# Kernel optimization log

Measured on AMD Instinct MI355X. Metric: run time of the kernel, lower is better.

The kernel has to match this reference:

```python
import jax, jax.numpy as jnp
import numpy as np

B, T, C, NH = 1, 2048, 1024, 16
HS = C // NH            # 64
LEVEL = 6
LMIN = 2 ** LEVEL       # 64 (tail block size)
NB = T // LMIN          # 32 complete sets


def setup_inputs() -> dict:
    key = jax.random.key(0)
    ks = jax.random.split(key, 8)
    def w(k, shape, fan_in):
        return jax.random.normal(k, shape, jnp.float32) / np.sqrt(fan_in)
    return {
        "x": jax.random.normal(ks[0], (B, T, C), jnp.float32),
        "Wq": w(ks[1], (C, C), C),
        "Wk": w(ks[2], (C, C), C),
        "Wv": w(ks[3], (C, C), C),
        "Wkmap": w(ks[4], (HS, HS * HS), HS * HS),
        "bkmap": jnp.zeros((HS,), jnp.float32),
        "Wvmap": w(ks[5], (HS, HS * HS), HS * HS),
        "bvmap": jnp.zeros((HS,), jnp.float32),
        "Wc": w(ks[6], (C, C), C),
        "bc": jnp.zeros((C,), jnp.float32),
    }


def reference(x, Wq, Wk, Wv, Wkmap, bkmap, Wvmap, bvmap, Wc, bc):
    phi = lambda t: jax.nn.elu(t) + 1.0  # feature_map='elu'
    # preprocess: projections + feature map (no q/k normalization)
    q = phi((x @ Wq.T).reshape(B, T, NH, HS))
    k = phi((x @ Wk.T).reshape(B, T, NH, HS))
    v = (x @ Wv.T).reshape(B, T, NH, HS)

    # per-position outer products k_t (x) v_t, grouped into LMIN-sized blocks
    op = jnp.einsum('bthd,bthe->bthde', k, v).reshape(B, NB, LMIN, NH, HS, HS)
    # set feature = final state of linear-attn recurrence over each full block
    set_f = op.sum(axis=2).reshape(B, NB, NH, HS * HS)            # [B,NB,NH,HS^2]
    # tail feature at t = state over [t - t%LMIN, t] = in-block prefix cumsum
    tail_f = jnp.cumsum(op, axis=2).reshape(B, T, NH, HS * HS)    # [B,T,NH,HS^2]

    K = set_f @ Wkmap.T + bkmap      # [B,NB,NH,HS] (k_mapping=True)
    V = set_f @ Wvmap.T + bvmap      # [B,NB,NH,HS] (v_mapping=True)
    K_tail = tail_f @ Wkmap.T + bkmap  # [B,T,NH,HS]
    V_tail = tail_f @ Wvmap.T + bvmap  # [B,T,NH,HS]

    scale = 1.0 / np.sqrt(HS)
    logits = jnp.einsum('bthd,bshd->bhts', q, K) * scale          # [B,NH,T,NB]
    # query t may attend only complete sets strictly before its own block
    mask = jnp.arange(NB)[None, :] < (jnp.arange(T) // LMIN)[:, None]  # [T,NB]
    logits = jnp.where(mask[None, None], logits, -jnp.inf)
    tail_logit = (jnp.einsum('bthd,bthd->bth', q, K_tail) * scale)
    tail_logit = tail_logit.transpose(0, 2, 1)[..., None]         # [B,NH,T,1]

    att = jax.nn.softmax(jnp.concatenate([logits, tail_logit], axis=-1), axis=-1)
    out = (jnp.einsum('bhts,bshd->bhtd', att[..., :-1], V)
           + att[..., -1:] * V_tail.transpose(0, 2, 1, 3))        # [B,NH,T,HS]
    out = out.transpose(0, 2, 1, 3).reshape(B, T, C)
    return out @ Wc.T + bc
```

## Files before the change

kernel.cpp:

```cpp
#include <hip/hip_runtime.h>
#include <hip/hip_bf16.h>
#include <math.h>

typedef __hip_bfloat16 bf16;
typedef __attribute__((ext_vector_type(8))) short short8;
typedef __attribute__((ext_vector_type(4))) float f32x4;

#define C_DIM 1024
#define NHEAD 16
#define HS 64

__device__ __forceinline__ float bf2f(bf16 x) { return __bfloat162float(x); }
__device__ __forceinline__ short bfbits(float x) {
    bf16 h = __float2bfloat16(x);
    return *reinterpret_cast<short*>(&h);
}

__device__ __forceinline__ void gl16(const void* g, void* l) {
    __builtin_amdgcn_global_load_lds(
        (const __attribute__((address_space(1))) unsigned int*)g,
        (__attribute__((address_space(3))) unsigned int*)l, 16, 0, 0);
}

__device__ __forceinline__ void split8(const float* p, short8& h, short8& l) {
    float4 f0 = reinterpret_cast<const float4*>(p)[0];
    float4 f1 = reinterpret_cast<const float4*>(p)[1];
    float vals[8] = {f0.x, f0.y, f0.z, f0.w, f1.x, f1.y, f1.z, f1.w};
#pragma unroll
    for (int j = 0; j < 8; ++j) {
        bf16 hb = __float2bfloat16(vals[j]);
        float r = vals[j] - __bfloat162float(hb);
        h[j] = *reinterpret_cast<short*>(&hb);
        bf16 lb = __float2bfloat16(r);
        l[j] = *reinterpret_cast<short*>(&lb);
    }
}

__device__ __forceinline__ short8* tchunk(bf16* tile, int row, int ch) {
    return reinterpret_cast<short8*>(tile + row * 64 + (((ch) ^ (row & 7)) << 3));
}

__global__ __launch_bounds__(256) void presplit_all_kernel(
    const float* __restrict__ x, const float* __restrict__ Wq,
    const float* __restrict__ Wk, const float* __restrict__ Wv,
    bf16* __restrict__ xh, bf16* __restrict__ xl,
    bf16* __restrict__ wqh, bf16* __restrict__ wql,
    bf16* __restrict__ wkh, bf16* __restrict__ wkl,
    bf16* __restrict__ wvh, bf16* __restrict__ wvl)
{
    int blk = blockIdx.x;
    const float* src; bf16 *dh, *dl; long off;
    if (blk < 1024)      { src = x;  dh = xh;  dl = xl;  off = (long)blk * 2048; }
    else if (blk < 1536) { src = Wq; dh = wqh; dl = wql; off = (long)(blk - 1024) * 2048; }
    else if (blk < 2048) { src = Wk; dh = wkh; dl = wkl; off = (long)(blk - 1536) * 2048; }
    else                 { src = Wv; dh = wvh; dl = wvl; off = (long)(blk - 2048) * 2048; }
    long p = off + threadIdx.x * 8;
    int j = (int)(((p >> 3) ^ (p >> 10)) & 7);
    long dp = (p & ~56l) | ((long)j << 3);
    short8 h8, l8;
    split8(&src[p], h8, l8);
    *reinterpret_cast<short8*>(&dh[dp]) = h8;
    *reinterpret_cast<short8*>(&dl[dp]) = l8;
}

__global__ __launch_bounds__(256) void presplit_wc_kernel(
    const float* __restrict__ Wc, bf16* __restrict__ wch, bf16* __restrict__ wcl)
{
    long p = (long)blockIdx.x * 2048 + threadIdx.x * 8;
    int j = (int)(((p >> 3) ^ (p >> 10)) & 7);
    long dp = (p & ~56l) | ((long)j << 3);
    short8 h8, l8;
    split8(&Wc[p], h8, l8);
    *reinterpret_cast<short8*>(&wch[dp]) = h8;
    *reinterpret_cast<short8*>(&wcl[dp]) = l8;
}

__global__ __launch_bounds__(256) void presplit_wmap_kernel(
    const float* __restrict__ WK, const float* __restrict__ WV, bf16* __restrict__ Wm4)
{
    int d = blockIdx.x;
    int row = threadIdx.x >> 2, e0 = (threadIdx.x & 3) * 16;
    int sw0 = (((e0 >> 3) + 0) ^ (row & 7)) & 7;
    int sw1 = (((e0 >> 3) + 1) ^ (row & 7)) & 7;
    const float* pk = &WK[(long)row * 4096 + d * 64 + e0];
    const float* pv = &WV[(long)row * 4096 + d * 64 + e0];
    long bKh = ((long)(d * 4 + 0) * 64 + row) * 64;
    long bKl = ((long)(d * 4 + 1) * 64 + row) * 64;
    long bVh = ((long)(d * 4 + 2) * 64 + row) * 64;
    long bVl = ((long)(d * 4 + 3) * 64 + row) * 64;
    short8 h8, l8;
    split8(pk, h8, l8);     *(short8*)&Wm4[bKh + sw0*8] = h8; *(short8*)&Wm4[bKl + sw0*8] = l8;
    split8(pk + 8, h8, l8); *(short8*)&Wm4[bKh + sw1*8] = h8; *(short8*)&Wm4[bKl + sw1*8] = l8;
    split8(pv, h8, l8);     *(short8*)&Wm4[bVh + sw0*8] = h8; *(short8*)&Wm4[bVl + sw0*8] = l8;
    split8(pv + 8, h8, l8); *(short8*)&Wm4[bVh + sw1*8] = h8; *(short8*)&Wm4[bVl + sw1*8] = l8;
}

__global__ __launch_bounds__(256) void qkv_kernel(
    const bf16* __restrict__ xh, const bf16* __restrict__ xl,
    const bf16* __restrict__ wqh, const bf16* __restrict__ wql,
    const bf16* __restrict__ wkh, const bf16* __restrict__ wkl,
    const bf16* __restrict__ wvh, const bf16* __restrict__ wvl,
    float* __restrict__ qkv)
{
    __shared__ bf16 lds[32768];
    const int tid = threadIdx.x;
    const int lane = tid & 63, wid = tid >> 6;
    const int wr = wid >> 1, wc = wid & 1;
    const int proj = blockIdx.x >> 3;
    const int n0 = (blockIdx.x & 7) * 128;
    const int m0 = blockIdx.y * 128;
    const bf16* Bhp = proj == 0 ? wqh : (proj == 1 ? wkh : wvh);
    const bf16* Blp = proj == 0 ? wql : (proj == 1 ? wkl : wvl);
    float* C = qkv + (long)proj * 2097152;
    char* lb = reinterpret_cast<char*>(lds);

    f32x4 acc[4][4] = {};
    for (int kt = 0; kt < 16; ++kt) {
        const int k0 = kt << 6;
#pragma unroll
        for (int i = 0; i < 4; ++i) {
            int cc = tid + i * 256;
            int row = cc >> 3, j = cc & 7;
            long soA = (long)(m0 + row) * 1024 + k0 + j * 8;
            long soB = (long)(n0 + row) * 1024 + k0 + j * 8;
            gl16(&xh[soA],  lb + cc * 16);
            gl16(&xl[soA],  lb + 16384 + cc * 16);
            gl16(&Bhp[soB], lb + 32768 + cc * 16);
            gl16(&Blp[soB], lb + 49152 + cc * 16);
        }
        __syncthreads();
#pragma unroll
        for (int kk = 0; kk < 2; ++kk) {
            short8 afh[4], afl[4], bfh[4], bfl[4];
#pragma unroll
            for (int t = 0; t < 4; ++t) {
                int ra = wr * 64 + t * 16 + (lane & 15);
                int rb = wc * 64 + t * 16 + (lane & 15);
                int ch = kk * 4 + (lane >> 4);
                afh[t] = *tchunk(lds, ra, ch);
                afl[t] = *tchunk(lds + 8192, ra, ch);
                bfh[t] = *tchunk(lds + 16384, rb, ch);
                bfl[t] = *tchunk(lds + 24576, rb, ch);
            }
#pragma unroll
            for (int tm = 0; tm < 4; ++tm)
#pragma unroll
                for (int tn = 0; tn < 4; ++tn) {
                    acc[tm][tn] = __builtin_amdgcn_mfma_f32_16x16x32_bf16(
                        afh[tm], bfh[tn], acc[tm][tn], 0, 0, 0);
                    acc[tm][tn] = __builtin_amdgcn_mfma_f32_16x16x32_bf16(
                        afh[tm], bfl[tn], acc[tm][tn], 0, 0, 0);
                    acc[tm][tn] = __builtin_amdgcn_mfma_f32_16x16x32_bf16(
                        afl[tm], bfh[tn], acc[tm][tn], 0, 0, 0);
                }
        }
        __syncthreads();
    }
#pragma unroll
    for (int tm = 0; tm < 4; ++tm)
#pragma unroll
        for (int tn = 0; tn < 4; ++tn)
#pragma unroll
            for (int r = 0; r < 4; ++r) {
                int row = m0 + wr * 64 + tm * 16 + (lane >> 4) * 4 + r;
                int col = n0 + wc * 64 + tn * 16 + (lane & 15);
                float v = acc[tm][tn][r];
                if (proj < 2) v = v > 0.f ? v + 1.f : __expf(v);
                C[(long)row * 1024 + col] = v;
            }
}

__global__ __launch_bounds__(512) void setfeat_kernel(
    const float* __restrict__ kbuf, const float* __restrict__ vbuf,
    const bf16* __restrict__ Wm4,
    const float* __restrict__ bkmap, const float* __restrict__ bvmap,
    float* __restrict__ Ktail, float* __restrict__ Vtail,
    float* __restrict__ KsetT, float* __restrict__ Vset)
{
    __shared__ char smem[98304];
    bf16* W0 = reinterpret_cast<bf16*>(smem);
    bf16* W1 = reinterpret_cast<bf16*>(smem + 32768);
    const int tid = threadIdx.x;
    const int grp = tid >> 8;
    const int tl = tid & 255;
    const int lane = tl & 63, wid = tl >> 6;
    const int wr = wid >> 1, wc = wid & 1;
    const int pairIdx = blockIdx.x * 2 + grp;
    const int b = pairIdx >> 4, h = pairIdx & 15;
    const long base_kv = ((long)b * 64) * C_DIM + h * HS;
    float* kT = reinterpret_cast<float*>(smem + 65536 + grp * 16384);

    {
        int s = tl >> 2, cg = tl & 3;
        const float* src = &kbuf[base_kv + (long)s * C_DIM + cg * 16];
        float f[16];
#pragma unroll
        for (int j = 0; j < 4; ++j)
            *reinterpret_cast<float4*>(&f[j * 4]) = reinterpret_cast<const float4*>(src)[j];
#pragma unroll
        for (int j = 0; j < 16; ++j)
            kT[(cg * 16 + j) * 64 + s] = f[j];
    }
    short8 vh[2][2];
#pragma unroll
    for (int tm = 0; tm < 2; ++tm)
#pragma unroll
        for (int kk = 0; kk < 2; ++kk) {
            const float* vp = &vbuf[base_kv +
                (long)(wr * 32 + tm * 16 + (lane & 15)) * C_DIM + kk * 32 + (lane >> 4) * 8];
            float4 f0 = reinterpret_cast<const float4*>(vp)[0];
            float4 f1 = reinterpret_cast<const float4*>(vp)[1];
            float vals[8] = {f0.x, f0.y, f0.z, f0.w, f1.x, f1.y, f1.z, f1.w};
#pragma unroll
            for (int j = 0; j < 8; ++j) vh[tm][kk][j] = bfbits(vals[j]);
        }
#pragma unroll
    for (int i = 0; i < 4; ++i) {
        int cc = tid + i * 512;
        gl16(&Wm4[(long)cc * 8], smem + (long)cc * 16);
    }
    f32x4 accK[2][2] = {}, accV[2][2] = {};
    __syncthreads();

    for (int d = 0; d < 64; ++d) {
        bf16* Wcur = (d & 1) ? W1 : W0;
        char* Wnxt = (d & 1) ? smem : smem + 32768;
        __builtin_amdgcn_s_barrier();
        if (d < 63) {
#pragma unroll
            for (int i = 0; i < 4; ++i) {
                int cc = tid + i * 512;
                gl16(&Wm4[(long)(d + 1) * 16384 + (long)cc * 8], Wnxt + (long)cc * 16);
            }
            asm volatile("s_waitcnt vmcnt(4)" ::: "memory");
        } else {
            asm volatile("s_waitcnt vmcnt(0)" ::: "memory");
        }
        f32x4 GK[2][2] = {}, GV[2][2] = {};
#pragma unroll
        for (int kk = 0; kk < 2; ++kk) {
            short8 bkh[2], bkl[2], bvh[2], bvl[2];
#pragma unroll
            for (int t = 0; t < 2; ++t) {
                int rb = wc * 32 + t * 16 + (lane & 15);
                int ch = kk * 4 + (lane >> 4);
                bkh[t] = *tchunk(Wcur,         rb, ch);
                bkl[t] = *tchunk(Wcur + 4096,  rb, ch);
                bvh[t] = *tchunk(Wcur + 8192,  rb, ch);
                bvl[t] = *tchunk(Wcur + 12288, rb, ch);
            }
#pragma unroll
            for (int tm = 0; tm < 2; ++tm)
#pragma unroll
                for (int tn = 0; tn < 2; ++tn) {
                    GK[tm][tn] = __builtin_amdgcn_mfma_f32_16x16x32_bf16(
                        vh[tm][kk], bkh[tn], GK[tm][tn], 0, 0, 0);
                    GK[tm][tn] = __builtin_amdgcn_mfma_f32_16x16x32_bf16(
                        vh[tm][kk], bkl[tn], GK[tm][tn], 0, 0, 0);
                    GV[tm][tn] = __builtin_amdgcn_mfma_f32_16x16x32_bf16(
                        vh[tm][kk], bvh[tn], GV[tm][tn], 0, 0, 0);
                    GV[tm][tn] = __builtin_amdgcn_mfma_f32_16x16x32_bf16(
                        vh[tm][kk], bvl[tn], GV[tm][tn], 0, 0, 0);
                }
        }
#pragma unroll
        for (int tm = 0; tm < 2; ++tm) {
            f32x4 kv = *reinterpret_cast<const f32x4*>(
                &kT[d * 64 + wr * 32 + tm * 16 + (lane >> 4) * 4]);
#pragma unroll
            for (int tn = 0; tn < 2; ++tn)
#pragma unroll
                for (int r = 0; r < 4; ++r) {
                    accK[tm][tn][r] += kv[r] * GK[tm][tn][r];
                    accV[tm][tn][r] += kv[r] * GV[tm][tn][r];
                }
        }
    }
    __syncthreads();
    float(*WallK)[64] = reinterpret_cast<float(*)[64]>(smem + grp * 32768);
    float(*WallV)[64] = reinterpret_cast<float(*)[64]>(smem + grp * 32768 + 16384);
#pragma unroll
    for (int tm = 0; tm < 2; ++tm)
#pragma unroll
        for (int tn = 0; tn < 2; ++tn)
#pragma unroll
            for (int r = 0; r < 4; ++r) {
                int row = wr * 32 + tm * 16 + (lane >> 4) * 4 + r;
                int col = wc * 32 + tn * 16 + (lane & 15);
                WallK[row][col] = accK[tm][tn][r];
                WallV[row][col] = accV[tm][tn][r];
            }
    __syncthreads();
    if (tl < 128) {
        int i = tl & 63;
        bool isV = tl >= 64;
        const float bi = isV ? bvmap[i] : bkmap[i];
        float run = 0.f;
        for (int s = 0; s < 64; ++s) {
            run += isV ? WallV[s][i] : WallK[s][i];
            float val = run + bi;
            long t = (long)b * 64 + s;
            if (isV) Vtail[t * C_DIM + h * HS + i] = val;
            else     Ktail[t * C_DIM + h * HS + i] = val;
            if (s == 63) {
                if (isV) Vset[(b * NHEAD + h) * HS + i] = val;
                else     KsetT[h * 2048 + i * 32 + b] = val;
            }
        }
    }
}

__global__ __launch_bounds__(256) void attn_kernel(
    const float* __restrict__ qbuf, const float* __restrict__ KsetT,
    const float* __restrict__ Vset, const float* __restrict__ Ktail,
    const float* __restrict__ Vtail, bf16* __restrict__ atth, bf16* __restrict__ attl)
{
    __shared__ float qsh[4][64];
    __shared__ float attsh[4][64];
    const int tid = threadIdx.x, lane = tid & 63, wid = tid >> 6;
    const int g = blockIdx.x * 4 + wid;
    const int t = g >> 4, h = g & 15;
    const int nb = t >> 6;
    const float scale = 0.125f;
    const long qoff = (long)t * C_DIM + h * HS;
    float qv = qbuf[qoff + lane];
    qsh[wid][lane] = qv;
    float tp = qv * Ktail[qoff + lane];
    for (int off = 32; off; off >>= 1) tp += __shfl_xor(tp, off, 64);
    __syncthreads();
    float logit = -INFINITY;
    if (lane < nb) {
        float s = 0.f;
        const float* Kp = &KsetT[h * 2048 + lane];
        for (int d = 0; d < 64; ++d) s += qsh[wid][d] * Kp[d * 32];
        logit = s * scale;
    } else if (lane == nb) {
        logit = tp * scale;
    }
    float m = logit;
    for (int off = 32; off; off >>= 1) m = fmaxf(m, __shfl_xor(m, off, 64));
    float e = (lane <= nb) ? __expf(logit - m) : 0.f;
    float sum = e;
    for (int off = 32; off; off >>= 1) sum += __shfl_xor(sum, off, 64);
    attsh[wid][lane] = e / sum;
    __syncthreads();
    float out = 0.f;
    for (int s = 0; s < nb; ++s)
        out += attsh[wid][s] * Vset[(s * NHEAD + h) * HS + lane];
    out += attsh[wid][nb] * Vtail[qoff + lane];
    bf16 hb = __float2bfloat16(out);
    int csw = (((lane >> 3) ^ (t & 7)) << 3) | (lane & 7);
    long po = (long)t * 1024 + h * 64 + csw;
    atth[po] = hb;
    attl[po] = __float2bfloat16(out - bf2f(hb));
}

__global__ __launch_bounds__(256) void gemm_final_kernel(
    const bf16* __restrict__ ah, const bf16* __restrict__ al,
    const bf16* __restrict__ bh, const bf16* __restrict__ bl,
    const float* __restrict__ bias, float* __restrict__ C)
{
    __shared__ bf16 lds[24576];
    const int tid = threadIdx.x;
    const int lane = tid & 63, wid = tid >> 6;
    const int wr = wid >> 1, wc = wid & 1;
    const int m0 = blockIdx.y * 128, n0 = blockIdx.x * 64;
    char* lb = reinterpret_cast<char*>(lds);

    f32x4 acc[4][2] = {};
    for (int kt = 0; kt < 16; ++kt) {
        const int k0 = kt << 6;
#pragma unroll
        for (int i = 0; i < 4; ++i) {
            int cc = tid + i * 256;
            int row = cc >> 3, j = cc & 7;
            long so = (long)(m0 + row) * 1024 + k0 + j * 8;
            gl16(&ah[so], lb + cc * 16);
            gl16(&al[so], lb + 16384 + cc * 16);
        }
#pragma unroll
        for (int i = 0; i < 2; ++i) {
            int cc = tid + i * 256;
            int row = cc >> 3, j = cc & 7;
            long so = (long)(n0 + row) * 1024 + k0 + j * 8;
            gl16(&bh[so], lb + 32768 + cc * 16);
            gl16(&bl[so], lb + 40960 + cc * 16);
        }
        __syncthreads();
#pragma unroll
        for (int kk = 0; kk < 2; ++kk) {
            short8 afh[4], afl[4], bfh[2], bfl[2];
#pragma unroll
            for (int t = 0; t < 4; ++t) {
                int ra = wr * 64 + t * 16 + (lane & 15);
                int ch = kk * 4 + (lane >> 4);
                afh[t] = *tchunk(lds, ra, ch);
                afl[t] = *tchunk(lds + 8192, ra, ch);
            }
#pragma unroll
            for (int t = 0; t < 2; ++t) {
                int rb = wc * 32 + t * 16 + (lane & 15);
                int ch = kk * 4 + (lane >> 4);
                bfh[t] = *tchunk(lds + 16384, rb, ch);
                bfl[t] = *tchunk(lds + 20480, rb, ch);
            }
#pragma unroll
            for (int tm = 0; tm < 4; ++tm)
#pragma unroll
                for (int tn = 0; tn < 2; ++tn) {
                    acc[tm][tn] = __builtin_amdgcn_mfma_f32_16x16x32_bf16(
                        afh[tm], bfh[tn], acc[tm][tn], 0, 0, 0);
                    acc[tm][tn] = __builtin_amdgcn_mfma_f32_16x16x32_bf16(
                        afh[tm], bfl[tn], acc[tm][tn], 0, 0, 0);
                    acc[tm][tn] = __builtin_amdgcn_mfma_f32_16x16x32_bf16(
                        afl[tm], bfh[tn], acc[tm][tn], 0, 0, 0);
                }
        }
        __syncthreads();
    }
#pragma unroll
    for (int tm = 0; tm < 4; ++tm)
#pragma unroll
        for (int tn = 0; tn < 2; ++tn)
#pragma unroll
            for (int r = 0; r < 4; ++r) {
                int row = m0 + wr * 64 + tm * 16 + (lane >> 4) * 4 + r;
                int col = n0 + wc * 32 + tn * 16 + (lane & 15);
                C[(long)row * 1024 + col] = acc[tm][tn][r] + bias[col];
            }
}

extern "C" void kernel_launch(void* const* d_in, const int* in_sizes, int n_in,
                              void* d_out, int out_size, void* d_ws, size_t ws_size,
                              hipStream_t stream)
{
    const float* x     = (const float*)d_in[0];
    const float* Wq    = (const float*)d_in[1];
    const float* Wk    = (const float*)d_in[2];
    const float* Wv    = (const float*)d_in[3];
    const float* Wkmap = (const float*)d_in[4];
    const float* bkmap = (const float*)d_in[5];
    const float* Wvmap = (const float*)d_in[6];
    const float* bvmap = (const float*)d_in[7];
    const float* Wc    = (const float*)d_in[8];
    const float* bc    = (const float*)d_in[9];
    float* out = (float*)d_out;

    char* ws = (char*)d_ws;
    const long MB = 1l << 20;
    float* q   = (float*)(ws + 0 * MB);
    float* k   = (float*)(ws + 8 * MB);
    float* v   = (float*)(ws + 16 * MB);
    bf16* xh   = (bf16*)(ws + 24 * MB);
    bf16* xl   = (bf16*)(ws + 28 * MB);
    bf16* wqh  = (bf16*)(ws + 32 * MB);
    bf16* wql  = (bf16*)(ws + 34 * MB);
    bf16* wkh  = (bf16*)(ws + 36 * MB);
    bf16* wkl  = (bf16*)(ws + 38 * MB);
    bf16* wvh  = (bf16*)(ws + 40 * MB);
    bf16* wvl  = (bf16*)(ws + 42 * MB);
    bf16* Wm4  = (bf16*)(ws + 44 * MB);
    float* Ktail = (float*)(ws + 24 * MB);
    float* Vtail = (float*)(ws + 32 * MB);
    float* KsetT = (float*)(ws + 40 * MB);
    float* Vset  = (float*)(ws + 41 * MB);
    bf16* atth   = (bf16*)(ws + 8 * MB);
    bf16* attl   = (bf16*)(ws + 12 * MB);
    bf16* wch    = (bf16*)(ws + 44 * MB);
    bf16* wcl    = (bf16*)(ws + 46 * MB);

    presplit_all_kernel<<<2560, 256, 0, stream>>>(x, Wq, Wk, Wv, xh, xl,
                                                  wqh, wql, wkh, wkl, wvh, wvl);
    presplit_wmap_kernel<<<64, 256, 0, stream>>>(Wkmap, Wvmap, Wm4);
    qkv_kernel<<<dim3(24, 16), 256, 0, stream>>>(xh, xl, wqh, wql, wkh, wkl,
                                                 wvh, wvl, q);
    setfeat_kernel<<<256, 512, 0, stream>>>(k, v, Wm4, bkmap, bvmap,
                                            Ktail, Vtail, KsetT, Vset);
    presplit_wc_kernel<<<512, 256, 0, stream>>>(Wc, wch, wcl);
    attn_kernel<<<8192, 256, 0, stream>>>(q, KsetT, Vset, Ktail, Vtail, atth, attl);
    gemm_final_kernel<<<dim3(16, 16), 256, 0, stream>>>(atth, attl, wch, wcl, bc, out);
}
```

Baseline: 257.0 us.

## Fold k scaling into MFMA operand and emit transposed k from QKV GEMM

The set-feature kernel used to compute per-d GEMM results G and then scale-accumulate them with k on the vector ALU. It now multiplies k[s,d] into the v operand before rounding to bf16 and accumulates straight into the MFMA accumulators, which removes the G temporaries and the FMA epilogue. The QKV kernel writes the k projection already transposed per (block, head) through a swizzled LDS staging buffer. That drops the in-kernel transpose and its LDS space, and launch bounds now target higher occupancy. The bf16 rounding now applies to the k·v product rather than to v alone, which slightly changes numerics.

After: 258.7 us. About the same (+0.7%).

```diff
diff --git a/kernel.cpp b/kernel.cpp
--- a/kernel.cpp
+++ b/kernel.cpp
@@ -100,7 +100,7 @@
     const bf16* __restrict__ wqh, const bf16* __restrict__ wql,
     const bf16* __restrict__ wkh, const bf16* __restrict__ wkl,
     const bf16* __restrict__ wvh, const bf16* __restrict__ wvl,
-    float* __restrict__ qkv)
+    float* __restrict__ qkv, float* __restrict__ kTg)
 {
     __shared__ bf16 lds[32768];
     const int tid = threadIdx.x;
@@ -156,87 +156,108 @@
         }
         __syncthreads();
     }
-#pragma unroll
-    for (int tm = 0; tm < 4; ++tm)
-#pragma unroll
-        for (int tn = 0; tn < 4; ++tn)
-#pragma unroll
-            for (int r = 0; r < 4; ++r) {
-                int row = m0 + wr * 64 + tm * 16 + (lane >> 4) * 4 + r;
-                int col = n0 + wc * 64 + tn * 16 + (lane & 15);
-                float v = acc[tm][tn][r];
-                if (proj < 2) v = v > 0.f ? v + 1.f : __expf(v);
-                C[(long)row * 1024 + col] = v;
-            }
-}
-
-__global__ __launch_bounds__(512) void setfeat_kernel(
-    const float* __restrict__ kbuf, const float* __restrict__ vbuf,
+    if (proj == 1) {
+        float* lf = reinterpret_cast<float*>(lds) + wid * 4096;
+#pragma unroll
+        for (int tm = 0; tm < 4; ++tm)
+#pragma unroll
+            for (int tn = 0; tn < 4; ++tn)
+#pragma unroll
+                for (int r = 0; r < 4; ++r) {
+                    int s = tm * 16 + (lane >> 4) * 4 + r;
+                    int dd = tn * 16 + (lane & 15);
+                    float v = acc[tm][tn][r];
+                    v = v > 0.f ? v + 1.f : __expf(v);
+                    lf[dd * 64 + (s ^ dd)] = v;
+                }
+        asm volatile("s_waitcnt lgkmcnt(0)" ::: "memory");
+        __builtin_amdgcn_sched_barrier(0);
+        int pair = (blockIdx.y * 2 + wr) * 16 + ((blockIdx.x & 7) * 2 + wc);
+        long pb = (long)pair * 4096;
+        int s0 = (lane & 15) * 4;
+#pragma unroll
+        for (int ii = 0; ii < 16; ++ii) {
+            int dd = (lane >> 4) * 16 + ii;
+            float4 o;
+            o.x = lf[dd * 64 + ((s0 + 0) ^ dd)];
+            o.y = lf[dd * 64 + ((s0 + 1) ^ dd)];
+            o.z = lf[dd * 64 + ((s0 + 2) ^ dd)];
+            o.w = lf[dd * 64 + ((s0 + 3) ^ dd)];
+            *reinterpret_cast<float4*>(&kTg[pb + (long)dd * 64 + s0]) = o;
+        }
+    } else {
+#pragma unroll
+        for (int tm = 0; tm < 4; ++tm)
+#pragma unroll
+            for (int tn = 0; tn < 4; ++tn)
+#pragma unroll
+                for (int r = 0; r < 4; ++r) {
+                    int row = m0 + wr * 64 + tm * 16 + (lane >> 4) * 4 + r;
+                    int col = n0 + wc * 64 + tn * 16 + (lane & 15);
+                    float v = acc[tm][tn][r];
+                    if (proj == 0) v = v > 0.f ? v + 1.f : __expf(v);
+                    C[(long)row * 1024 + col] = v;
+                }
+    }
+}
+
+__global__ __launch_bounds__(512, 4) void setfeat_kernel(
+    const float* __restrict__ kTg, const float* __restrict__ vbuf,
     const bf16* __restrict__ Wm4,
     const float* __restrict__ bkmap, const float* __restrict__ bvmap,
     float* __restrict__ Ktail, float* __restrict__ Vtail,
     float* __restrict__ KsetT, float* __restrict__ Vset)
 {
-    __shared__ char smem[98304];
+    __shared__ char smem[65536];
     bf16* W0 = reinterpret_cast<bf16*>(smem);
     bf16* W1 = reinterpret_cast<bf16*>(smem + 32768);
     const int tid = threadIdx.x;
-    const int grp = tid >> 8;
-    const int tl = tid & 255;
+    const int grp = tid >> 8, tl = tid & 255;
     const int lane = tl & 63, wid = tl >> 6;
     const int wr = wid >> 1, wc = wid & 1;
     const int pairIdx = blockIdx.x * 2 + grp;
     const int b = pairIdx >> 4, h = pairIdx & 15;
     const long base_kv = ((long)b * 64) * C_DIM + h * HS;
-    float* kT = reinterpret_cast<float*>(smem + 65536 + grp * 16384);
-
-    {
-        int s = tl >> 2, cg = tl & 3;
-        const float* src = &kbuf[base_kv + (long)s * C_DIM + cg * 16];
-        float f[16];
-#pragma unroll
-        for (int j = 0; j < 4; ++j)
-            *reinterpret_cast<float4*>(&f[j * 4]) = reinterpret_cast<const float4*>(src)[j];
-#pragma unroll
-        for (int j = 0; j < 16; ++j)
-            kT[(cg * 16 + j) * 64 + s] = f[j];
-    }
-    short8 vh[2][2];
-#pragma unroll
-    for (int tm = 0; tm < 2; ++tm)
-#pragma unroll
-        for (int kk = 0; kk < 2; ++kk) {
-            const float* vp = &vbuf[base_kv +
-                (long)(wr * 32 + tm * 16 + (lane & 15)) * C_DIM + kk * 32 + (lane >> 4) * 8];
-            float4 f0 = reinterpret_cast<const float4*>(vp)[0];
-            float4 f1 = reinterpret_cast<const float4*>(vp)[1];
-            float vals[8] = {f0.x, f0.y, f0.z, f0.w, f1.x, f1.y, f1.z, f1.w};
-#pragma unroll
-            for (int j = 0; j < 8; ++j) vh[tm][kk][j] = bfbits(vals[j]);
-        }
+    const float* kp = kTg + (long)pairIdx * 4096;
+
+    float vv0[2][8], vv1[2][8];
+#pragma unroll
+    for (int kk = 0; kk < 2; ++kk) {
+        const float* p0 = &vbuf[base_kv +
+            (long)(wr * 32 + (lane & 15)) * C_DIM + kk * 32 + (lane >> 4) * 8];
+        const float* p1 = &vbuf[base_kv +
+            (long)(wr * 32 + 16 + (lane & 15)) * C_DIM + kk * 32 + (lane >> 4) * 8];
+        *reinterpret_cast<float4*>(&vv0[kk][0]) = reinterpret_cast<const float4*>(p0)[0];
+        *reinterpret_cast<float4*>(&vv0[kk][4]) = reinterpret_cast<const float4*>(p0)[1];
+        *reinterpret_cast<float4*>(&vv1[kk][0]) = reinterpret_cast<const float4*>(p1)[0];
+        *reinterpret_cast<float4*>(&vv1[kk][4]) = reinterpret_cast<const float4*>(p1)[1];
+    }
+    float ks0 = kp[wr * 32 + (lane & 15)];
+    float ks1 = kp[wr * 32 + 16 + (lane & 15)];
 #pragma unroll
     for (int i = 0; i < 4; ++i) {
         int cc = tid + i * 512;
         gl16(&Wm4[(long)cc * 8], smem + (long)cc * 16);
     }
     f32x4 accK[2][2] = {}, accV[2][2] = {};
-    __syncthreads();
 
     for (int d = 0; d < 64; ++d) {
         bf16* Wcur = (d & 1) ? W1 : W0;
         char* Wnxt = (d & 1) ? smem : smem + 32768;
         __builtin_amdgcn_s_barrier();
+        float kn0 = 0.f, kn1 = 0.f;
         if (d < 63) {
+            kn0 = kp[(d + 1) * 64 + wr * 32 + (lane & 15)];
+            kn1 = kp[(d + 1) * 64 + wr * 32 + 16 + (lane & 15)];
 #pragma unroll
             for (int i = 0; i < 4; ++i) {
                 int cc = tid + i * 512;
                 gl16(&Wm4[(long)(d + 1) * 16384 + (long)cc * 8], Wnxt + (long)cc * 16);
             }
-            asm volatile("s_waitcnt vmcnt(4)" ::: "memory");
+            asm volatile("s_waitcnt vmcnt(6)" ::: "memory");
         } else {
             asm volatile("s_waitcnt vmcnt(0)" ::: "memory");
         }
-        f32x4 GK[2][2] = {}, GV[2][2] = {};
 #pragma unroll
         for (int kk = 0; kk < 2; ++kk) {
             short8 bkh[2], bkl[2], bvh[2], bvl[2];
@@ -249,32 +270,25 @@
                 bvh[t] = *tchunk(Wcur + 8192,  rb, ch);
                 bvl[t] = *tchunk(Wcur + 12288, rb, ch);
             }
-#pragma unroll
-            for (int tm = 0; tm < 2; ++tm)
-#pragma unroll
-                for (int tn = 0; tn < 2; ++tn) {
-                    GK[tm][tn] = __builtin_amdgcn_mfma_f32_16x16x32_bf16(
-                        vh[tm][kk], bkh[tn], GK[tm][tn], 0, 0, 0);
-                    GK[tm][tn] = __builtin_amdgcn_mfma_f32_16x16x32_bf16(
-                        vh[tm][kk], bkl[tn], GK[tm][tn], 0, 0, 0);
-                    GV[tm][tn] = __builtin_amdgcn_mfma_f32_16x16x32_bf16(
-                        vh[tm][kk], bvh[tn], GV[tm][tn], 0, 0, 0);
-                    GV[tm][tn] = __builtin_amdgcn_mfma_f32_16x16x32_bf16(
-                        vh[tm][kk], bvl[tn], GV[tm][tn], 0, 0, 0);
-                }
-        }
-#pragma unroll
-        for (int tm = 0; tm < 2; ++tm) {
-            f32x4 kv = *reinterpret_cast<const f32x4*>(
-                &kT[d * 64 + wr * 32 + tm * 16 + (lane >> 4) * 4]);
-#pragma unroll
-            for (int tn = 0; tn < 2; ++tn)
-#pragma unroll
-                for (int r = 0; r < 4; ++r) {
-                    accK[tm][tn][r] += kv[r] * GK[tm][tn][r];
-                    accV[tm][tn][r] += kv[r] * GV[tm][tn][r];
-                }
-        }
+            short8 a0, a1;
+#pragma unroll
+            for (int j = 0; j < 8; ++j) {
+                a0[j] = bfbits(ks0 * vv0[kk][j]);
+                a1[j] = bfbits(ks1 * vv1[kk][j]);
+            }
+#pragma unroll
+            for (int tn = 0; tn < 2; ++tn) {
+                accK[0][tn] = __builtin_amdgcn_mfma_f32_16x16x32_bf16(a0, bkh[tn], accK[0][tn], 0, 0, 0);
+                accK[0][tn] = __builtin_amdgcn_mfma_f32_16x16x32_bf16(a0, bkl[tn], accK[0][tn], 0, 0, 0);
+                accK[1][tn] = __builtin_amdgcn_mfma_f32_16x16x32_bf16(a1, bkh[tn], accK[1][tn], 0, 0, 0);
+                accK[1][tn] = __builtin_amdgcn_mfma_f32_16x16x32_bf16(a1, bkl[tn], accK[1][tn], 0, 0, 0);
+                accV[0][tn] = __builtin_amdgcn_mfma_f32_16x16x32_bf16(a0, bvh[tn], accV[0][tn], 0, 0, 0);
+                accV[0][tn] = __builtin_amdgcn_mfma_f32_16x16x32_bf16(a0, bvl[tn], accV[0][tn], 0, 0, 0);
+                accV[1][tn] = __builtin_amdgcn_mfma_f32_16x16x32_bf16(a1, bvh[tn], accV[1][tn], 0, 0, 0);
+                accV[1][tn] = __builtin_amdgcn_mfma_f32_16x16x32_bf16(a1, bvl[tn], accV[1][tn], 0, 0, 0);
+            }
+        }
+        ks0 = kn0; ks1 = kn1;
     }
     __syncthreads();
     float(*WallK)[64] = reinterpret_cast<float(*)[64]>(smem + grp * 32768);
@@ -287,8 +301,8 @@
             for (int r = 0; r < 4; ++r) {
                 int row = wr * 32 + tm * 16 + (lane >> 4) * 4 + r;
                 int col = wc * 32 + tn * 16 + (lane & 15);
-                WallK[row][col] = accK[tm][tn][r];
-                WallV[row][col] = accV[tm][tn][r];
+                WallK[row][col] = (tm == 0 ? accK[0][tn][r] : accK[1][tn][r]);
+                WallV[row][col] = (tm == 0 ? accV[0][tn][r] : accV[1][tn][r]);
             }
     __syncthreads();
     if (tl < 128) {
@@ -449,7 +463,7 @@
     char* ws = (char*)d_ws;
     const long MB = 1l << 20;
     float* q   = (float*)(ws + 0 * MB);
-    float* k   = (float*)(ws + 8 * MB);
+    float* kTg = (float*)(ws + 8 * MB);
     float* v   = (float*)(ws + 16 * MB);
     bf16* xh   = (bf16*)(ws + 24 * MB);
     bf16* xl   = (bf16*)(ws + 28 * MB);
@@ -473,8 +487,8 @@
                                                   wqh, wql, wkh, wkl, wvh, wvl);
     presplit_wmap_kernel<<<64, 256, 0, stream>>>(Wkmap, Wvmap, Wm4);
     qkv_kernel<<<dim3(24, 16), 256, 0, stream>>>(xh, xl, wqh, wql, wkh, wkl,
-                                                 wvh, wvl, q);
-    setfeat_kernel<<<256, 512, 0, stream>>>(k, v, Wm4, bkmap, bvmap,
+                                                 wvh, wvl, q, kTg);
+    setfeat_kernel<<<256, 512, 0, stream>>>(kTg, v, Wm4, bkmap, bvmap,
                                             Ktail, Vtail, KsetT, Vset);
     presplit_wc_kernel<<<512, 256, 0, stream>>>(Wc, wch, wcl);
     attn_kernel<<<8192, 256, 0, stream>>>(q, KsetT, Vset, Ktail, Vtail, atth, attl);
```
